# Kernel tuning notes

Hardware: AMD Instinct MI355X
Metric: run time of the kernel (lower is better)

Reference implementation:

```python
import jax, jax.numpy as jnp
import numpy as np

SEQ_LEN, BATCH, TAG = 512, 1024, 64
START_IDX, END_IDX = 0, 1
NEG_INF = -10000.0


def setup_inputs() -> dict:
    key = jax.random.key(0)
    k1, k2, k3 = jax.random.split(key, 3)
    feats = jax.random.normal(k1, (SEQ_LEN, BATCH, TAG), dtype=jnp.float32)
    # variable-length sequences: valid prefix lengths in [SEQ_LEN//2, SEQ_LEN]
    lens = jax.random.randint(k2, (BATCH,), SEQ_LEN // 2, SEQ_LEN + 1)
    mask = (jnp.arange(SEQ_LEN)[:, None] < lens[None, :]).astype(jnp.float32)  # (S, B)
    # transition ~ xavier_normal_ then clamp START row / END column (reset_parameters)
    std = float(np.sqrt(2.0 / (TAG + TAG)))
    transition = jax.random.normal(k3, (TAG, TAG), dtype=jnp.float32) * std
    transition = transition.at[START_IDX, :].set(NEG_INF)
    transition = transition.at[:, END_IDX].set(NEG_INF)
    return {"feats": feats, "mask": mask, "transition": transition}


def reference(feats, mask, transition):
    # feats: (S, B, T), mask: (S, B), transition: (T, T) [next_tag, prev_tag]
    S, B, T = feats.shape
    alpha0 = jnp.full((B, T), NEG_INF, dtype=feats.dtype).at[:, START_IDX].set(0.0)

    def step(alpha, xs):
        feat, m = xs  # feat: (B, T), m: (B,)
        # alpha_score[b, next, prev] = alpha[b, prev] + transition[next, prev] + feat[b, next]
        score = alpha[:, None, :] + transition[None, :, :] + feat[:, :, None]
        new_alpha = jax.nn.logsumexp(score, axis=-1)  # (B, T)
        m = m[:, None]
        alpha = new_alpha * m + alpha * (1.0 - m)
        return alpha, None

    alpha, _ = jax.lax.scan(step, alpha0, (feats, mask))
    alpha = alpha + transition[END_IDX][None, :]
    return jax.nn.logsumexp(alpha, axis=-1)  # (B,)
```

## Files before the change

kernel.cpp:

```cpp
#include <hip/hip_runtime.h>

namespace {
constexpr int S_LEN = 512;
constexpr int BATCH = 1024;
constexpr int TAG = 64;
constexpr int START_IDX = 0;
constexpr int END_IDX = 1;
constexpr float NEG_INF = -10000.0f;
constexpr int CHUNK = 64;
constexpr float LN2F = 0.69314718055994530942f;

typedef float v2f __attribute__((ext_vector_type(2)));
typedef float v4f __attribute__((ext_vector_type(4)));

typedef const __attribute__((address_space(1))) void* gas_ptr;
typedef __attribute__((address_space(3))) void* las_ptr;

__device__ inline void gld_lds16(const float* g, float* l) {
  __builtin_amdgcn_global_load_lds((gas_ptr)(const void*)g, (las_ptr)(void*)l, 16, 0, 0);
}
}

__global__ __launch_bounds__(64, 1) void crf_fwd_kernel(
    const float* __restrict__ feats,
    const float* __restrict__ mask,
    const float* __restrict__ trans,
    float* __restrict__ out) {
  const int b = blockIdx.x;
  const int lane = threadIdx.x;

  __shared__ __align__(16) float fchunk[2][CHUNK * TAG];

  int L;
  {
    float sum = 0.0f;
#pragma unroll
    for (int k = 0; k < S_LEN / 64; ++k) sum += mask[(size_t)(lane + 64 * k) * BATCH + b];
#pragma unroll
    for (int off = 32; off >= 1; off >>= 1) sum += __shfl_xor(sum, off, 64);
    L = (int)(sum + 0.5f);
  }

  float Ee[TAG];
  {
    const float* row = trans + lane * TAG;
#pragma unroll
    for (int k = 0; k < TAG / 4; ++k) {
      v4f tv;
      __builtin_memcpy(&tv, row + 4 * k, sizeof(v4f));
      Ee[4 * k + 0] = __expf(tv.x);
      Ee[4 * k + 1] = __expf(tv.y);
      Ee[4 * k + 2] = __expf(tv.z);
      Ee[4 * k + 3] = __expf(tv.w);
    }
  }

  const float* gstage0 =
      feats + ((size_t)(lane >> 4) * BATCH + b) * TAG + ((lane & 15) << 2);

  auto stage_chunk = [&](int base_s, int nb) {
    const float* g0 = gstage0 + (size_t)base_s * (BATCH * TAG);
#pragma unroll
    for (int q = 0; q < 16; ++q) {
      gld_lds16(g0 + (size_t)(4 * q) * (BATCH * TAG), &fchunk[nb][q * 256]);
    }
  };

  float p = (lane == START_IDX) ? 1.0f : 0.0f;
  int etot = 0;

  stage_chunk(0, 0);
  asm volatile("s_waitcnt vmcnt(0)" ::: "memory");
  __builtin_amdgcn_sched_barrier(0);
  __builtin_amdgcn_wave_barrier();

  auto step = [&](float ex) {
    const unsigned pu = __float_as_uint(p);

    const unsigned pb = __builtin_amdgcn_readlane(pu, 2);
    const unsigned eb = (pb == 0u) ? 127u : (pb >> 23);
    etot += (int)eb - 127;
    const float scale = __uint_as_float((254u - eb) << 23);
    const float cg = ex * scale;

    float a0 = 0.f, a1 = 0.f, a2 = 0.f, a3 = 0.f;
    float a4 = 0.f, a5 = 0.f, a6 = 0.f, a7 = 0.f;
#pragma unroll
    for (int k = 0; k < TAG; k += 8) {
      a0 = __builtin_fmaf(__uint_as_float(__builtin_amdgcn_readlane(pu, k + 0)), Ee[k + 0], a0);
      a1 = __builtin_fmaf(__uint_as_float(__builtin_amdgcn_readlane(pu, k + 1)), Ee[k + 1], a1);
      a2 = __builtin_fmaf(__uint_as_float(__builtin_amdgcn_readlane(pu, k + 2)), Ee[k + 2], a2);
      a3 = __builtin_fmaf(__uint_as_float(__builtin_amdgcn_readlane(pu, k + 3)), Ee[k + 3], a3);
      a4 = __builtin_fmaf(__uint_as_float(__builtin_amdgcn_readlane(pu, k + 4)), Ee[k + 4], a4);
      a5 = __builtin_fmaf(__uint_as_float(__builtin_amdgcn_readlane(pu, k + 5)), Ee[k + 5], a5);
      a6 = __builtin_fmaf(__uint_as_float(__builtin_amdgcn_readlane(pu, k + 6)), Ee[k + 6], a6);
      a7 = __builtin_fmaf(__uint_as_float(__builtin_amdgcn_readlane(pu, k + 7)), Ee[k + 7], a7);
    }
    const float t = ((a0 + a1) + (a2 + a3)) + ((a4 + a5) + (a6 + a7));
    p = t * cg;
  };

  for (int c = 0;; ++c) {
    const int base = c * CHUNK;
    int n = L - base;
    if (n <= 0) break;
    if (n > CHUNK) n = CHUNK;

    const int nbase = base + CHUNK;
    if (nbase < S_LEN) stage_chunk(nbase, (c + 1) & 1);

    const float* fb = &fchunk[c & 1][0];

    auto group8 = [&](int s0) {
      float ex[8];
#pragma unroll
      for (int i = 0; i < 8; ++i) ex[i] = fb[(s0 + i) * TAG + lane];
#pragma unroll
      for (int i = 0; i < 8; ++i) ex[i] = __expf(ex[i]);
#pragma unroll
      for (int i = 0; i < 8; ++i) step(ex[i]);
    };

    if (n == CHUNK) {
      for (int g = 0; g < CHUNK / 8; ++g) group8(8 * g);
    } else {
      const int full = n >> 3;
      for (int g = 0; g < full; ++g) group8(8 * g);
      for (int i = full * 8; i < n; ++i) {
        step(__expf(fb[i * TAG + lane]));
      }
      break;
    }

    if (nbase >= L) break;

    asm volatile("s_waitcnt vmcnt(0)" ::: "memory");
    __builtin_amdgcn_sched_barrier(0);
    __builtin_amdgcn_wave_barrier();
  }

  asm volatile("s_waitcnt vmcnt(0)" ::: "memory");

  {
    const float a = (float)etot * LN2F + __logf(p) + trans[END_IDX * TAG + lane];
    float mx = a;
#pragma unroll
    for (int off = 32; off >= 1; off >>= 1) mx = fmaxf(mx, __shfl_xor(mx, off, 64));
    float e = __expf(a - mx);
#pragma unroll
    for (int off = 32; off >= 1; off >>= 1) e += __shfl_xor(e, off, 64);
    if (lane == 0) out[b] = mx + __logf(e);
  }
}

extern "C" void kernel_launch(void* const* d_in, const int* in_sizes, int n_in,
                              void* d_out, int out_size, void* d_ws, size_t ws_size,
                              hipStream_t stream) {
  const float* feats = (const float*)d_in[0];
  const float* mask = (const float*)d_in[1];
  const float* trans = (const float*)d_in[2];
  float* out = (float*)d_out;
  crf_fwd_kernel<<<dim3(BATCH), dim3(64), 0, stream>>>(feats, mask, trans, out);
}
```

Before: 271.6 us.

## Split tag matvec across lane quads with LDS broadcast and packed FMA

Replaces the per-step scheme, where each lane reads all 64 alpha values through readlane, with a layout where each lane computes a 16-element partial dot product for 4 next-tags. The previous alpha comes from LDS as vector loads, the math uses packed v2f multiply-adds, and partials are reduced within each quad using DPP swaps. Each step then writes the new alpha back to LDS. The aim is to cut the serial chain of 64 readlanes per step, at the cost of an LDS write/read round trip and DPP latency on the critical path.

```diff
diff --git a/kernel.cpp b/kernel.cpp
--- a/kernel.cpp
+++ b/kernel.cpp
@@ -6,7 +6,6 @@
 constexpr int TAG = 64;
 constexpr int START_IDX = 0;
 constexpr int END_IDX = 1;
-constexpr float NEG_INF = -10000.0f;
 constexpr int CHUNK = 64;
 constexpr float LN2F = 0.69314718055994530942f;
 
@@ -18,6 +17,12 @@
 
 __device__ inline void gld_lds16(const float* g, float* l) {
   __builtin_amdgcn_global_load_lds((gas_ptr)(const void*)g, (las_ptr)(void*)l, 16, 0, 0);
+}
+
+template <int CTRL>
+__device__ __forceinline__ float qswap(float v) {
+  return __uint_as_float((unsigned)__builtin_amdgcn_mov_dpp(
+      (int)__float_as_uint(v), CTRL, 0xF, 0xF, false));
 }
 }
 
@@ -28,8 +33,11 @@
     float* __restrict__ out) {
   const int b = blockIdx.x;
   const int lane = threadIdx.x;
+  const int q = lane >> 2;
+  const int c = lane & 3;
 
   __shared__ __align__(16) float fchunk[2][CHUNK * TAG];
+  __shared__ __align__(16) float p_lds[TAG];
 
   int L;
   {
@@ -41,17 +49,16 @@
     L = (int)(sum + 0.5f);
   }
 
-  float Ee[TAG];
-  {
-    const float* row = trans + lane * TAG;
-#pragma unroll
-    for (int k = 0; k < TAG / 4; ++k) {
+  v2f El[4][8];
+#pragma unroll
+  for (int m = 0; m < 4; ++m) {
+    const float* row = trans + (size_t)(4 * q + m) * TAG + 16 * c;
+#pragma unroll
+    for (int k = 0; k < 4; ++k) {
       v4f tv;
       __builtin_memcpy(&tv, row + 4 * k, sizeof(v4f));
-      Ee[4 * k + 0] = __expf(tv.x);
-      Ee[4 * k + 1] = __expf(tv.y);
-      Ee[4 * k + 2] = __expf(tv.z);
-      Ee[4 * k + 3] = __expf(tv.w);
+      El[m][2 * k]     = v2f{__expf(tv.x), __expf(tv.y)};
+      El[m][2 * k + 1] = v2f{__expf(tv.z), __expf(tv.w)};
     }
   }
 
@@ -61,12 +68,14 @@
   auto stage_chunk = [&](int base_s, int nb) {
     const float* g0 = gstage0 + (size_t)base_s * (BATCH * TAG);
 #pragma unroll
-    for (int q = 0; q < 16; ++q) {
-      gld_lds16(g0 + (size_t)(4 * q) * (BATCH * TAG), &fchunk[nb][q * 256]);
+    for (int t = 0; t < 16; ++t) {
+      gld_lds16(g0 + (size_t)(4 * t) * (BATCH * TAG), &fchunk[nb][t * 256]);
     }
   };
 
-  float p = (lane == START_IDX) ? 1.0f : 0.0f;
+  p_lds[lane] = (lane == START_IDX) ? 1.0f : 0.0f;
+  __builtin_amdgcn_wave_barrier();
+  float pm0 = (q == 0) ? 1.0f : 0.0f, pm1 = 0.0f, pm2 = 0.0f, pm3 = 0.0f;
   int etot = 0;
 
   stage_chunk(0, 0);
@@ -74,60 +83,96 @@
   __builtin_amdgcn_sched_barrier(0);
   __builtin_amdgcn_wave_barrier();
 
-  auto step = [&](float ex) {
-    const unsigned pu = __float_as_uint(p);
-
-    const unsigned pb = __builtin_amdgcn_readlane(pu, 2);
+  auto step = [&](const v4f& cgv) {
+    const unsigned pb = __builtin_amdgcn_readlane(__float_as_uint(pm2), 0);
     const unsigned eb = (pb == 0u) ? 127u : (pb >> 23);
     etot += (int)eb - 127;
     const float scale = __uint_as_float((254u - eb) << 23);
-    const float cg = ex * scale;
-
-    float a0 = 0.f, a1 = 0.f, a2 = 0.f, a3 = 0.f;
-    float a4 = 0.f, a5 = 0.f, a6 = 0.f, a7 = 0.f;
-#pragma unroll
-    for (int k = 0; k < TAG; k += 8) {
-      a0 = __builtin_fmaf(__uint_as_float(__builtin_amdgcn_readlane(pu, k + 0)), Ee[k + 0], a0);
-      a1 = __builtin_fmaf(__uint_as_float(__builtin_amdgcn_readlane(pu, k + 1)), Ee[k + 1], a1);
-      a2 = __builtin_fmaf(__uint_as_float(__builtin_amdgcn_readlane(pu, k + 2)), Ee[k + 2], a2);
-      a3 = __builtin_fmaf(__uint_as_float(__builtin_amdgcn_readlane(pu, k + 3)), Ee[k + 3], a3);
-      a4 = __builtin_fmaf(__uint_as_float(__builtin_amdgcn_readlane(pu, k + 4)), Ee[k + 4], a4);
-      a5 = __builtin_fmaf(__uint_as_float(__builtin_amdgcn_readlane(pu, k + 5)), Ee[k + 5], a5);
-      a6 = __builtin_fmaf(__uint_as_float(__builtin_amdgcn_readlane(pu, k + 6)), Ee[k + 6], a6);
-      a7 = __builtin_fmaf(__uint_as_float(__builtin_amdgcn_readlane(pu, k + 7)), Ee[k + 7], a7);
-    }
-    const float t = ((a0 + a1) + (a2 + a3)) + ((a4 + a5) + (a6 + a7));
-    p = t * cg;
+    const float cg0 = cgv.x * scale, cg1 = cgv.y * scale;
+    const float cg2 = cgv.z * scale, cg3 = cgv.w * scale;
+
+    const float* pl = p_lds + 16 * c;
+    v4f r0, r1, r2, r3;
+    __builtin_memcpy(&r0, pl + 0,  sizeof(v4f));
+    __builtin_memcpy(&r1, pl + 4,  sizeof(v4f));
+    __builtin_memcpy(&r2, pl + 8,  sizeof(v4f));
+    __builtin_memcpy(&r3, pl + 12, sizeof(v4f));
+    const v2f pv0 = {r0.x, r0.y}, pv1 = {r0.z, r0.w};
+    const v2f pv2 = {r1.x, r1.y}, pv3 = {r1.z, r1.w};
+    const v2f pv4 = {r2.x, r2.y}, pv5 = {r2.z, r2.w};
+    const v2f pv6 = {r3.x, r3.y}, pv7 = {r3.z, r3.w};
+
+    float s0, s1, s2, s3;
+#pragma unroll
+    for (int m = 0; m < 4; ++m) {
+      v2f a = pv0 * El[m][0];
+      v2f d = pv1 * El[m][1];
+      a += pv2 * El[m][2];
+      d += pv3 * El[m][3];
+      a += pv4 * El[m][4];
+      d += pv5 * El[m][5];
+      a += pv6 * El[m][6];
+      d += pv7 * El[m][7];
+      const v2f t = a + d;
+      const float sm = t.x + t.y;
+      if (m == 0) s0 = sm; else if (m == 1) s1 = sm; else if (m == 2) s2 = sm; else s3 = sm;
+    }
+
+    s0 += qswap<0xB1>(s0);
+    s1 += qswap<0xB1>(s1);
+    s2 += qswap<0xB1>(s2);
+    s3 += qswap<0xB1>(s3);
+    s0 += qswap<0x4E>(s0);
+    s1 += qswap<0x4E>(s1);
+    s2 += qswap<0x4E>(s2);
+    s3 += qswap<0x4E>(s3);
+
+    pm0 = s0 * cg0;
+    pm1 = s1 * cg1;
+    pm2 = s2 * cg2;
+    pm3 = s3 * cg3;
+
+    __builtin_amdgcn_wave_barrier();
+    const v4f pw = {pm0, pm1, pm2, pm3};
+    __builtin_memcpy(&p_lds[4 * q], &pw, sizeof(v4f));
+    __builtin_amdgcn_wave_barrier();
   };
 
-  for (int c = 0;; ++c) {
-    const int base = c * CHUNK;
+  auto exp4 = [](v4f v) -> v4f {
+    return v4f{__expf(v.x), __expf(v.y), __expf(v.z), __expf(v.w)};
+  };
+
+  for (int ch = 0;; ++ch) {
+    const int base = ch * CHUNK;
     int n = L - base;
     if (n <= 0) break;
     if (n > CHUNK) n = CHUNK;
 
     const int nbase = base + CHUNK;
-    if (nbase < S_LEN) stage_chunk(nbase, (c + 1) & 1);
-
-    const float* fb = &fchunk[c & 1][0];
-
-    auto group8 = [&](int s0) {
-      float ex[8];
-#pragma unroll
-      for (int i = 0; i < 8; ++i) ex[i] = fb[(s0 + i) * TAG + lane];
-#pragma unroll
-      for (int i = 0; i < 8; ++i) ex[i] = __expf(ex[i]);
-#pragma unroll
-      for (int i = 0; i < 8; ++i) step(ex[i]);
+    if (nbase < S_LEN) stage_chunk(nbase, (ch + 1) & 1);
+
+    const float* fb = &fchunk[ch & 1][0];
+
+    auto group4 = [&](int s0g) {
+      v4f cg[4];
+#pragma unroll
+      for (int i = 0; i < 4; ++i)
+        __builtin_memcpy(&cg[i], fb + (s0g + i) * TAG + 4 * q, sizeof(v4f));
+#pragma unroll
+      for (int i = 0; i < 4; ++i) cg[i] = exp4(cg[i]);
+#pragma unroll
+      for (int i = 0; i < 4; ++i) step(cg[i]);
     };
 
     if (n == CHUNK) {
-      for (int g = 0; g < CHUNK / 8; ++g) group8(8 * g);
+      for (int g = 0; g < CHUNK / 4; ++g) group4(4 * g);
     } else {
-      const int full = n >> 3;
-      for (int g = 0; g < full; ++g) group8(8 * g);
-      for (int i = full * 8; i < n; ++i) {
-        step(__expf(fb[i * TAG + lane]));
+      const int full = n >> 2;
+      for (int g = 0; g < full; ++g) group4(4 * g);
+      for (int i = full * 4; i < n; ++i) {
+        v4f cg;
+        __builtin_memcpy(&cg, fb + i * TAG + 4 * q, sizeof(v4f));
+        step(exp4(cg));
       }
       break;
     }
@@ -142,7 +187,9 @@
   asm volatile("s_waitcnt vmcnt(0)" ::: "memory");
 
   {
-    const float a = (float)etot * LN2F + __logf(p) + trans[END_IDX * TAG + lane];
+    __builtin_amdgcn_wave_barrier();
+    const float pj = p_lds[lane];
+    const float a = (float)etot * LN2F + __logf(pj) + trans[END_IDX * TAG + lane];
     float mx = a;
 #pragma unroll
     for (int off = 32; off >= 1; off >>= 1) mx = fmaxf(mx, __shfl_xor(mx, off, 64));
```

New measurement: 268.9 us. Within noise of the previous version (-1.0%).
